# Kernel tuning notes

Hardware: AMD Instinct MI355X
Metric: run time of the kernel (lower is better)

The kernel has to match this reference:

```python
import jax, jax.numpy as jnp
import numpy as np

B, T, C = 4, 2048, 1024
N_HEADS = 16
HEAD_DIM = C // N_HEADS


def setup_inputs() -> dict:
    key = jax.random.key(0)
    k1, k2, k3, k4, k5 = jax.random.split(key, 5)
    x = jax.random.normal(k1, (B, T, C), dtype=jnp.float32)
    # torch Linear: y = x @ W.T + b; store W as [out, in]
    w_qkv = jax.random.normal(k2, (3 * C, C), dtype=jnp.float32) * (1.0 / np.sqrt(C))
    b_qkv = jax.random.normal(k3, (3 * C,), dtype=jnp.float32) * 0.01
    w_proj = jax.random.normal(k4, (C, C), dtype=jnp.float32) * (1.0 / np.sqrt(C))
    b_proj = jax.random.normal(k5, (C,), dtype=jnp.float32) * 0.01
    return {"x": x, "w_qkv": w_qkv, "b_qkv": b_qkv, "w_proj": w_proj, "b_proj": b_proj}


def reference(x, w_qkv, b_qkv, w_proj, b_proj):
    Bx, Tx, Cx = x.shape
    scale = 1.0 / np.sqrt(HEAD_DIM)
    qkv = x @ w_qkv.T + b_qkv                              # [B,T,3C]
    qkv = qkv.reshape(Bx, Tx, 3, N_HEADS, HEAD_DIM)
    qkv = jnp.transpose(qkv, (2, 0, 3, 1, 4))              # [3,B,H,T,D]
    q, k, v = qkv[0], qkv[1], qkv[2]
    att = jnp.einsum('bhqd,bhkd->bhqk', q, k) * scale      # [B,H,T,T]
    causal = jnp.tril(jnp.ones((Tx, Tx), dtype=bool))
    att = jnp.where(causal[None, None, :, :], att, -jnp.inf)
    att = jax.nn.softmax(att, axis=-1)
    # dropout p=0.0 (eval) -> identity
    out = jnp.einsum('bhqk,bhkd->bhqd', att, v)            # [B,H,T,D]
    out = jnp.transpose(out, (0, 2, 1, 3)).reshape(Bx, Tx, Cx)
    return out @ w_proj.T + b_proj
```

## Files before the change

### kernel.cpp

```cpp
#include <hip/hip_runtime.h>
#include <hip/hip_bf16.h>
#include <cstdint>

typedef __attribute__((ext_vector_type(8))) short bf16x8;
typedef __attribute__((ext_vector_type(4))) float f32x4;
typedef __attribute__((ext_vector_type(16))) float f32x16;

#define MFMA16(a, b, c) __builtin_amdgcn_mfma_f32_16x16x32_bf16(a, b, c, 0, 0, 0)
#define MFMA32(a, b, c) __builtin_amdgcn_mfma_f32_32x32x16_bf16(a, b, c, 0, 0, 0)

typedef __attribute__((address_space(1))) uint32_t as1_u32;
typedef __attribute__((address_space(3))) uint32_t as3_u32;
static __device__ __forceinline__ void gload16(const void* g, void* l) {
  __builtin_amdgcn_global_load_lds((as1_u32*)g, (as3_u32*)l, 16, 0, 0);
}

static __device__ __forceinline__ ushort f2b(float f) {
  union { float f; uint32_t u; } v; v.f = f;
  uint32_t u = v.u;
  uint32_t r = (u + 0x7FFFu + ((u >> 16) & 1u)) >> 16;
  return (ushort)r;
}

static __device__ __forceinline__ uint32_t cvtpk(float a, float b) {
  uint32_t r;
  asm("v_cvt_pk_bf16_f32 %0, %1, %2" : "=v"(r) : "v"(a), "v"(b));
  return r;
}
static __device__ __forceinline__ void plswap(uint32_t& a, uint32_t& b) {
  asm volatile("v_permlane32_swap_b32 %0, %1" : "+v"(a), "+v"(b));
}

#define QSCALE 0.1803368782f

__global__ void cvt_f32_bf16(const float* __restrict__ in, ushort* __restrict__ out, int n4) {
  int i = blockIdx.x * blockDim.x + threadIdx.x;
  if (i >= n4) return;
  const float4 v = ((const float4*)in)[i];
  ushort4 o;
  o.x = f2b(v.x); o.y = f2b(v.y); o.z = f2b(v.z); o.w = f2b(v.w);
  ((ushort4*)out)[i] = o;
}

template<int EPI>
__global__ __launch_bounds__(256) void gemm_bt(
    const ushort* __restrict__ A,
    const ushort* __restrict__ W,
    const float* __restrict__ bias,
    int M, int N, int K,
    ushort* __restrict__ q_ws, ushort* __restrict__ k_ws, ushort* __restrict__ v_ws,
    float* __restrict__ out) {
  __shared__ ushort As[3][64 * 64];
  __shared__ ushort Bs[3][64 * 64];
  const int tid = threadIdx.x;
  const int nbx = N >> 7;
  const int cpx = gridDim.x >> 3;
  const int wg = (blockIdx.x & 7) * cpx + (blockIdx.x >> 3);
  const int m0 = (wg / nbx) * 128, n0 = (wg % nbx) * 128;
  const int lane = tid & 63, w = tid >> 6;
  const int lr = lane & 15, lg = lane >> 4;
  const int wm = (w >> 1) * 64, wn = (w & 1) * 64;
  f32x4 acc[4][4] = {};

  const int nt = K >> 5;

#define GSTAGE(buf_, kt_)                                                   \
  do {                                                                      \
    const ushort* Asrc = A + (size_t)m0 * K + (kt_) * 32;                   \
    const ushort* Bsrc = W + (size_t)n0 * K + (kt_) * 32;                   \
    _Pragma("unroll") for (int i_ = 0; i_ < 2; ++i_) {                      \
      const int ch = i_ * 256 + tid;                            \
      const int prow = ch >> 3, pchk = ch & 7;                              \
      const int lchk = pchk ^ (prow & 7);              \
      const int r = prow * 2 + (lchk >> 2), kc = (lchk & 3) * 8;            \
      gload16(&Asrc[(size_t)r * K + kc], &As[buf_][ch * 8]);                \
      gload16(&Bsrc[(size_t)r * K + kc], &Bs[buf_][ch * 8]);                \
    }                                                                       \
  } while (0)

  GSTAGE(0, 0);
  GSTAGE(1, 1);
  asm volatile("s_waitcnt vmcnt(4)" ::: "memory");
  __builtin_amdgcn_s_barrier();
  asm volatile("" ::: "memory");

  int bcur = 0, bnxt = 2;
  for (int t = 0; t < nt; ++t) {
    if (t + 2 < nt) GSTAGE(bnxt, t + 2);
    const ushort* Asc = As[bcur];
    const ushort* Bsc = Bs[bcur];
    bf16x8 a[4], b[4];
#pragma unroll
    for (int mi = 0; mi < 4; ++mi) {
      const int r = wm + mi * 16 + lr;
      a[mi] = *(const bf16x8*)&Asc[(r >> 1) * 64 + (((((r & 1) << 2) | lg) ^ ((r >> 1) & 7)) * 8)];
    }
#pragma unroll
    for (int ni = 0; ni < 4; ++ni) {
      const int r = wn + ni * 16 + lr;
      b[ni] = *(const bf16x8*)&Bsc[(r >> 1) * 64 + (((((r & 1) << 2) | lg) ^ ((r >> 1) & 7)) * 8)];
    }
    __builtin_amdgcn_s_setprio(1);
#pragma unroll
    for (int mi = 0; mi < 4; ++mi)
#pragma unroll
      for (int ni = 0; ni < 4; ++ni)
        acc[mi][ni] = MFMA16(a[mi], b[ni], acc[mi][ni]);
    __builtin_amdgcn_s_setprio(0);
    if (t + 2 < nt)
      asm volatile("s_waitcnt vmcnt(4)" ::: "memory");
    else if (t + 1 < nt)
      asm volatile("s_waitcnt vmcnt(0)" ::: "memory");
    if (t + 1 < nt) {
      __builtin_amdgcn_s_barrier();
      asm volatile("" ::: "memory");
    }
    bcur = (bcur == 2) ? 0 : bcur + 1;
    bnxt = (bnxt == 2) ? 0 : bnxt + 1;
  }
#undef GSTAGE

#pragma unroll
  for (int mi = 0; mi < 4; ++mi) {
#pragma unroll
    for (int ni = 0; ni < 4; ++ni) {
      const int rowb = m0 + wm + mi * 16 + lg * 4;
      const int col = n0 + wn + ni * 16 + lr;
      float v[4];
#pragma unroll
      for (int i = 0; i < 4; ++i) v[i] = acc[mi][ni][i] + bias[col];
      if (EPI == 0) {
        const int sel = col >> 10;
        const int rem = col & 1023;
        const int h = rem >> 6, d = rem & 63;
        const int bb = rowb >> 11, t0 = rowb & 2047;
        if (sel == 2) {
          ushort4 st;
          st.x = f2b(v[0]); st.y = f2b(v[1]); st.z = f2b(v[2]); st.w = f2b(v[3]);
          *(ushort4*)&v_ws[((size_t)(bb * 16 + h) * 64 + d) * 2048 + t0] = st;
        } else if (sel == 0) {
#pragma unroll
          for (int i = 0; i < 4; ++i)
            q_ws[((size_t)(bb * 16 + h) * 2048 + t0 + i) * 64 + d] = f2b(v[i] * QSCALE);
        } else {
#pragma unroll
          for (int i = 0; i < 4; ++i)
            k_ws[((size_t)(bb * 16 + h) * 2048 + t0 + i) * 64 + d] = f2b(v[i]);
        }
      } else {
#pragma unroll
        for (int i = 0; i < 4; ++i)
          out[(size_t)(rowb + i) * N + col] = v[i];
      }
    }
  }
}

__global__ __launch_bounds__(256) void attn_v5(
    const ushort* __restrict__ Q, const ushort* __restrict__ K,
    const ushort* __restrict__ VT, ushort* __restrict__ O ) {
  const int blk = blockIdx.x;
  const int bh = blk & 63;
  const int pr = blk >> 6;
  const int tid = threadIdx.x;
  const int w = tid >> 6, lane = tid & 63;
  const int l31 = lane & 31, l5 = lane >> 5;
  const int bb = bh >> 4, h = bh & 15;
  const size_t base = (size_t)bh * 2048 * 64;
  const ushort* Qb = Q + base;
  const ushort* Kb = K + base;
  const ushort* VTb = VT + base;

  __shared__ ushort Ks[2][64 * 64];
  __shared__ ushort Vs[2][64 * 64];
  __shared__ float l_lds[4][32];

#define STAGE(buf, kt_)                                              \
  do {                                                               \
    const ushort* Kt = Kb + (size_t)(kt_) * 64 * 64;                 \
    const ushort* Vt = VTb + (kt_) * 64;                             \
    _Pragma("unroll") for (int i_ = 0; i_ < 2; ++i_) {               \
      const int ch = i_ * 256 + tid;                                 \
      const int r = ch >> 3;                                         \
      const int csw = ((ch & 7) ^ (r & 7)) * 8;                      \
      gload16(&Kt[(size_t)r * 64 + csw], &Ks[buf][ch * 8]);          \
      gload16(&Vt[(size_t)r * 2048 + csw], &Vs[buf][ch * 8]);        \
    }                                                                \
  } while (0)

#pragma unroll 1
  for (int ph = 0; ph < 2; ++ph) {
    const int s = ph ? pr : 15 - pr;
    const int q0w = s * 128 + w * 32;
    const int nt = 2 * s + 2;
    const int qlane = q0w + l31;

    bf16x8 qf[4];
#pragma unroll
    for (int dblk = 0; dblk < 4; ++dblk)
      qf[dblk] = *(const bf16x8*)&Qb[(size_t)qlane * 64 + dblk * 16 + l5 * 8];

    f32x16 o0 = {}, o1 = {};
    float lsum = 0.f;

    STAGE(0, 0);
    __syncthreads();

    for (int kt = 0; kt < nt; ++kt) {
      const int cur = kt & 1;
      if (kt + 1 < nt) STAGE(cur ^ 1, kt + 1);
      const int k0 = kt << 6;
      const ushort* Ksc = Ks[cur];
      const ushort* Vsc = Vs[cur];
#pragma unroll
      for (int kblk = 0; kblk < 2; ++kblk) {
        const int kbase = k0 + kblk * 32;
        if (kbase <= q0w + 31) {
          f32x16 st = {};
          __builtin_amdgcn_s_setprio(1);
#pragma unroll
          for (int dblk = 0; dblk < 4; ++dblk) {
            const int row = kblk * 32 + l31;
            bf16x8 ka = *(const bf16x8*)&Ksc[row * 64 + (((dblk * 2 + l5) ^ (row & 7)) * 8)];
            st = MFMA32(ka, qf[dblk], st);
          }
          __builtin_amdgcn_s_setprio(0);
          if (kbase + 31 > q0w) {
#pragma unroll
            for (int r = 0; r < 16; ++r) {
              const int kk = kbase + (r & 3) + 8 * (r >> 2) + 4 * l5;
              st[r] = (kk <= qlane) ? st[r] : -INFINITY;
            }
          }
          float p[16];
#pragma unroll
          for (int r = 0; r < 16; ++r) {
            p[r] = __builtin_amdgcn_exp2f(st[r]);
            lsum += p[r];
          }
#pragma unroll
          for (int sbl = 0; sbl < 2; ++sbl) {
            uint32_t P0 = cvtpk(p[8 * sbl + 0], p[8 * sbl + 1]);
            uint32_t P1 = cvtpk(p[8 * sbl + 2], p[8 * sbl + 3]);
            uint32_t P2 = cvtpk(p[8 * sbl + 4], p[8 * sbl + 5]);
            uint32_t P3 = cvtpk(p[8 * sbl + 6], p[8 * sbl + 7]);
            plswap(P0, P2);
            plswap(P1, P3);
            union { uint32_t u[4]; bf16x8 v; } pk;
            pk.u[0] = P0; pk.u[1] = P1; pk.u[2] = P2; pk.u[3] = P3;
            const int kchunk = kblk * 4 + sbl * 2 + l5;
            __builtin_amdgcn_s_setprio(1);
#pragma unroll
            for (int db2 = 0; db2 < 2; ++db2) {
              const int vrow = db2 * 32 + l31;
              bf16x8 vb = *(const bf16x8*)&Vsc[vrow * 64 + ((kchunk ^ (vrow & 7)) * 8)];
              if (db2 == 0) o0 = MFMA32(pk.v, vb, o0);
              else          o1 = MFMA32(pk.v, vb, o1);
            }
            __builtin_amdgcn_s_setprio(0);
          }
        }
      }
      __syncthreads();
    }

    const float lfull = lsum + __shfl_xor(lsum, 32);
    if (lane < 32) l_lds[w][lane] = 1.f / lfull;
#pragma unroll
    for (int r = 0; r < 16; ++r) {
      const int qoff = (r & 3) + 8 * (r >> 2) + 4 * l5;
      const float inv = l_lds[w][qoff];
      const int t = q0w + qoff;
      ushort* op = &O[(size_t)(bb * 2048 + t) * 1024 + h * 64 + l31];
      op[0] = f2b(o0[r] * inv);
      op[32] = f2b(o1[r] * inv);
    }
  }
#undef STAGE
}

extern "C" void kernel_launch(void* const* d_in, const int* in_sizes, int n_in,
                              void* d_out, int out_size, void* d_ws, size_t ws_size,
                              hipStream_t stream) {
  const float* x = (const float*)d_in[0];
  const float* w_qkv = (const float*)d_in[1];
  const float* b_qkv = (const float*)d_in[2];
  const float* w_proj = (const float*)d_in[3];
  const float* b_proj = (const float*)d_in[4];
  float* out = (float*)d_out;

  char* ws = (char*)d_ws;
  const size_t SZ_X = (size_t)8192 * 1024 * 2;
  const size_t SZ_WQ = (size_t)3072 * 1024 * 2;
  const size_t SZ_WP = (size_t)1024 * 1024 * 2;
  ushort* xb = (ushort*)(ws);
  ushort* wqb = (ushort*)(ws + SZ_X);
  ushort* wpb = (ushort*)(ws + SZ_X + SZ_WQ);
  ushort* q_ws = (ushort*)(ws + SZ_X + SZ_WQ + SZ_WP);
  ushort* k_ws = q_ws + (size_t)8192 * 1024;
  ushort* v_ws = k_ws + (size_t)8192 * 1024;

  cvt_f32_bf16<<<8388608 / 4 / 256, 256, 0, stream>>>(x, xb, 8388608 / 4);
  cvt_f32_bf16<<<3145728 / 4 / 256, 256, 0, stream>>>(w_qkv, wqb, 3145728 / 4);
  cvt_f32_bf16<<<1048576 / 4 / 256, 256, 0, stream>>>(w_proj, wpb, 1048576 / 4);

  gemm_bt<0><<<1536, 256, 0, stream>>>(
      xb, wqb, b_qkv, 8192, 3072, 1024, q_ws, k_ws, v_ws, nullptr);

  attn_v5<<<512, 256, 0, stream>>>(q_ws, k_ws, v_ws, xb);

  gemm_bt<1><<<512, 256, 0, stream>>>(
      xb, wpb, b_proj, 8192, 1024, 1024, nullptr, nullptr, nullptr, out);
}
```

Measured before the change: 169.8 us.

## Use 256x256-tile 8-wave QKV GEMM with phased staggered loads

Replaces the QKV projection GEMM with a dedicated kernel that uses 256x256 output tiles, 512 threads (8 waves) and K-steps of 64. Each K-step is split into four phases whose global-to-LDS loads for the next tiles are interleaved with MFMA work and separated by barriers. The larger tile raises arithmetic intensity and cuts global traffic per FLOP. In exchange it uses more LDS and registers (acc[8][4] per wave) and adds barriers per K-step. The projection GEMM is split out as its own non-templated kernel and is otherwise unchanged.

```diff
diff --git a/kernel.cpp b/kernel.cpp
--- a/kernel.cpp
+++ b/kernel.cpp
@@ -32,6 +32,8 @@
 }
 
 #define QSCALE 0.1803368782f
+
+#define LOFF(r, kc4) (((r) >> 1) * 64 + ((((((r) & 1) << 2) | (kc4)) ^ (((r) >> 1) & 7)) * 8))
 
 __global__ void cvt_f32_bf16(const float* __restrict__ in, ushort* __restrict__ out, int n4) {
   int i = blockIdx.x * blockDim.x + threadIdx.x;
@@ -42,13 +44,141 @@
   ((ushort4*)out)[i] = o;
 }
 
-template<int EPI>
-__global__ __launch_bounds__(256) void gemm_bt(
+__global__ __launch_bounds__(512, 2) void gemm_qkv_8ph(
     const ushort* __restrict__ A,
     const ushort* __restrict__ W,
     const float* __restrict__ bias,
     int M, int N, int K,
-    ushort* __restrict__ q_ws, ushort* __restrict__ k_ws, ushort* __restrict__ v_ws,
+    ushort* __restrict__ q_ws, ushort* __restrict__ k_ws, ushort* __restrict__ v_ws) {
+  __shared__ ushort As[2][2][2][64 * 64];
+  __shared__ ushort Bs[2][2][2][64 * 64];
+  const int tid = threadIdx.x;
+  const int nbx = N >> 8;
+  const int cpx = gridDim.x >> 3;
+  const int wg = (blockIdx.x & 7) * cpx + (blockIdx.x >> 3);
+  const int m0 = (wg / nbx) * 256, n0 = (wg % nbx) * 256;
+  const int wid = tid >> 6, lane = tid & 63;
+  const int wr = wid >> 2, wc = wid & 3;
+  const int lr = lane & 15, lg = lane >> 4;
+  const int prow = tid >> 3, pchk = tid & 7;
+  const int lchk = pchk ^ (prow & 7);
+  const int srow = prow * 2 + (lchk >> 2);
+  const int skc = (lchk & 3) * 8;
+
+  f32x4 acc[8][4] = {};
+  const int nt = K >> 6;
+
+#define STA(db_, half_, kt_)                                                  \
+  { const ushort* src = A + (size_t)(m0 + (half_)*128 + srow) * K + (kt_)*64 + skc; \
+    gload16(src, &As[db_][half_][0][tid * 8]);                                \
+    gload16(src + 32, &As[db_][half_][1][tid * 8]); }
+#define STB(db_, half_, kt_)                                                  \
+  { const ushort* src = W + (size_t)(n0 + (half_)*128 + srow) * K + (kt_)*64 + skc; \
+    gload16(src, &Bs[db_][half_][0][tid * 8]);                                \
+    gload16(src + 32, &Bs[db_][half_][1][tid * 8]); }
+
+  STB(0, 0, 0); STB(0, 1, 0);
+  STA(0, 0, 0); STA(0, 1, 0);
+  STB(1, 0, 1); STB(1, 1, 1);
+  asm volatile("s_waitcnt vmcnt(4)" ::: "memory");
+  __builtin_amdgcn_s_barrier();
+
+  for (int T = 0; T < nt; ++T) {
+    const int db = T & 1;
+    const ushort* A0 = &As[db][wr][0][0];
+    const ushort* A1 = &As[db][wr][1][0];
+    const ushort* B0 = &Bs[db][wc >> 1][0][0];
+    const ushort* B1 = &Bs[db][wc >> 1][1][0];
+    const int brow = (wc & 1) * 64;
+    bf16x8 b[4][2];
+#pragma unroll
+    for (int q = 0; q < 4; ++q) {
+      bf16x8 a[2][2];
+#pragma unroll
+      for (int mm = 0; mm < 2; ++mm) {
+        const int r = (2 * q + mm) * 16 + lr;
+        a[mm][0] = *(const bf16x8*)&A0[LOFF(r, lg)];
+        a[mm][1] = *(const bf16x8*)&A1[LOFF(r, lg)];
+      }
+      if (q == 0) {
+#pragma unroll
+        for (int nf = 0; nf < 4; ++nf) {
+          const int r = brow + nf * 16 + lr;
+          b[nf][0] = *(const bf16x8*)&B0[LOFF(r, lg)];
+          b[nf][1] = *(const bf16x8*)&B1[LOFF(r, lg)];
+        }
+      }
+      if (q == 0) {
+        if (T + 1 < nt) { STA((T + 1) & 1, 0, T + 1); STA((T + 1) & 1, 1, T + 1); }
+      } else if (q == 1) {
+        if (T + 2 < nt) STB(T & 1, 0, T + 2);
+      } else if (q == 2) {
+        if (T + 2 < nt) STB(T & 1, 1, T + 2);
+      }
+      __builtin_amdgcn_sched_barrier(0);
+      __builtin_amdgcn_s_barrier();
+      asm volatile("s_waitcnt lgkmcnt(0)" ::: "memory");
+      __builtin_amdgcn_sched_barrier(0);
+      __builtin_amdgcn_s_setprio(1);
+#pragma unroll
+      for (int kk = 0; kk < 2; ++kk)
+#pragma unroll
+        for (int mm = 0; mm < 2; ++mm)
+#pragma unroll
+          for (int nf = 0; nf < 4; ++nf)
+            acc[2 * q + mm][nf] = MFMA16(a[mm][kk], b[nf][kk], acc[2 * q + mm][nf]);
+      __builtin_amdgcn_s_setprio(0);
+      if (q == 3) {
+        if (T + 1 < nt) {
+          if (T + 2 < nt)
+            asm volatile("s_waitcnt vmcnt(4)" ::: "memory");
+          else
+            asm volatile("s_waitcnt vmcnt(0)" ::: "memory");
+          __builtin_amdgcn_s_barrier();
+        }
+      } else {
+        __builtin_amdgcn_s_barrier();
+      }
+    }
+  }
+#undef STA
+#undef STB
+
+#pragma unroll
+  for (int mf = 0; mf < 8; ++mf) {
+#pragma unroll
+    for (int nf = 0; nf < 4; ++nf) {
+      const int rowb = m0 + wr * 128 + mf * 16 + lg * 4;
+      const int col = n0 + wc * 64 + nf * 16 + lr;
+      float v[4];
+#pragma unroll
+      for (int i = 0; i < 4; ++i) v[i] = acc[mf][nf][i] + bias[col];
+      const int sel = col >> 10;
+      const int rem = col & 1023;
+      const int h = rem >> 6, d = rem & 63;
+      const int bb = rowb >> 11, t0 = rowb & 2047;
+      if (sel == 2) {
+        ushort4 st;
+        st.x = f2b(v[0]); st.y = f2b(v[1]); st.z = f2b(v[2]); st.w = f2b(v[3]);
+        *(ushort4*)&v_ws[((size_t)(bb * 16 + h) * 64 + d) * 2048 + t0] = st;
+      } else if (sel == 0) {
+#pragma unroll
+        for (int i = 0; i < 4; ++i)
+          q_ws[((size_t)(bb * 16 + h) * 2048 + t0 + i) * 64 + d] = f2b(v[i] * QSCALE);
+      } else {
+#pragma unroll
+        for (int i = 0; i < 4; ++i)
+          k_ws[((size_t)(bb * 16 + h) * 2048 + t0 + i) * 64 + d] = f2b(v[i]);
+      }
+    }
+  }
+}
+
+__global__ __launch_bounds__(256) void gemm_proj(
+    const ushort* __restrict__ A,
+    const ushort* __restrict__ W,
+    const float* __restrict__ bias,
+    int M, int N, int K,
     float* __restrict__ out) {
   __shared__ ushort As[3][64 * 64];
   __shared__ ushort Bs[3][64 * 64];
@@ -69,9 +199,9 @@
     const ushort* Asrc = A + (size_t)m0 * K + (kt_) * 32;                   \
     const ushort* Bsrc = W + (size_t)n0 * K + (kt_) * 32;                   \
     _Pragma("unroll") for (int i_ = 0; i_ < 2; ++i_) {                      \
-      const int ch = i_ * 256 + tid;                            \
+      const int ch = i_ * 256 + tid;                                        \
       const int prow = ch >> 3, pchk = ch & 7;                              \
-      const int lchk = pchk ^ (prow & 7);              \
+      const int lchk = pchk ^ (prow & 7);                                   \
       const int r = prow * 2 + (lchk >> 2), kc = (lchk & 3) * 8;            \
       gload16(&Asrc[(size_t)r * K + kc], &As[buf_][ch * 8]);                \
       gload16(&Bsrc[(size_t)r * K + kc], &Bs[buf_][ch * 8]);                \
@@ -93,12 +223,12 @@
 #pragma unroll
     for (int mi = 0; mi < 4; ++mi) {
       const int r = wm + mi * 16 + lr;
-      a[mi] = *(const bf16x8*)&Asc[(r >> 1) * 64 + (((((r & 1) << 2) | lg) ^ ((r >> 1) & 7)) * 8)];
+      a[mi] = *(const bf16x8*)&Asc[LOFF(r, lg)];
     }
 #pragma unroll
     for (int ni = 0; ni < 4; ++ni) {
       const int r = wn + ni * 16 + lr;
-      b[ni] = *(const bf16x8*)&Bsc[(r >> 1) * 64 + (((((r & 1) << 2) | lg) ^ ((r >> 1) & 7)) * 8)];
+      b[ni] = *(const bf16x8*)&Bsc[LOFF(r, lg)];
     }
     __builtin_amdgcn_s_setprio(1);
 #pragma unroll
@@ -126,32 +256,9 @@
     for (int ni = 0; ni < 4; ++ni) {
       const int rowb = m0 + wm + mi * 16 + lg * 4;
       const int col = n0 + wn + ni * 16 + lr;
-      float v[4];
-#pragma unroll
-      for (int i = 0; i < 4; ++i) v[i] = acc[mi][ni][i] + bias[col];
-      if (EPI == 0) {
-        const int sel = col >> 10;
-        const int rem = col & 1023;
-        const int h = rem >> 6, d = rem & 63;
-        const int bb = rowb >> 11, t0 = rowb & 2047;
-        if (sel == 2) {
-          ushort4 st;
-          st.x = f2b(v[0]); st.y = f2b(v[1]); st.z = f2b(v[2]); st.w = f2b(v[3]);
-          *(ushort4*)&v_ws[((size_t)(bb * 16 + h) * 64 + d) * 2048 + t0] = st;
-        } else if (sel == 0) {
-#pragma unroll
-          for (int i = 0; i < 4; ++i)
-            q_ws[((size_t)(bb * 16 + h) * 2048 + t0 + i) * 64 + d] = f2b(v[i] * QSCALE);
-        } else {
-#pragma unroll
-          for (int i = 0; i < 4; ++i)
-            k_ws[((size_t)(bb * 16 + h) * 2048 + t0 + i) * 64 + d] = f2b(v[i]);
-        }
-      } else {
-#pragma unroll
-        for (int i = 0; i < 4; ++i)
-          out[(size_t)(rowb + i) * N + col] = v[i];
-      }
+#pragma unroll
+      for (int i = 0; i < 4; ++i)
+        out[(size_t)(rowb + i) * N + col] = acc[mi][ni][i] + bias[col];
     }
   }
 }
@@ -304,11 +411,11 @@
   cvt_f32_bf16<<<3145728 / 4 / 256, 256, 0, stream>>>(w_qkv, wqb, 3145728 / 4);
   cvt_f32_bf16<<<1048576 / 4 / 256, 256, 0, stream>>>(w_proj, wpb, 1048576 / 4);
 
-  gemm_bt<0><<<1536, 256, 0, stream>>>(
-      xb, wqb, b_qkv, 8192, 3072, 1024, q_ws, k_ws, v_ws, nullptr);
+  gemm_qkv_8ph<<<384, 512, 0, stream>>>(
+      xb, wqb, b_qkv, 8192, 3072, 1024, q_ws, k_ws, v_ws);
 
   attn_v5<<<512, 256, 0, stream>>>(q_ws, k_ws, v_ws, xb);
 
-  gemm_bt<1><<<512, 256, 0, stream>>>(
-      xb, wpb, b_proj, 8192, 1024, 1024, nullptr, nullptr, nullptr, out);
-}
+  gemm_proj<<<512, 256, 0, stream>>>(
+      xb, wpb, b_proj, 8192, 1024, 1024, out);
+}
```

Measured after the change: 174.4 us. 1.03x slower.
